# Optimization experiments

Hardware: AMD Instinct MI355X
Metric: run time of the kernel (lower is better)

The kernel has to match this reference:

```python
import jax, jax.numpy as jnp
import numpy as np

SHAPES = ((100, 100), (50, 50), (25, 25), (13, 13))
LENS = [h * w for h, w in SHAPES]
STARTS = [0]
for n in LENS[:-1]:
    STARTS.append(STARTS[-1] + n)
S_TOT = sum(LENS)  # 13294
B, C, HH, DH, L, P, NQ, NL, FF = 2, 256, 8, 32, 4, 4, 300, 6, 1024
WH = np.array([[w, h] for h, w in SHAPES], np.float32)  # [L,2] (W,H) offset normalizer


def ln(x, g, b):
    m = x.mean(-1, keepdims=True)
    v = ((x - m) ** 2).mean(-1, keepdims=True)
    return (x - m) * jax.lax.rsqrt(v + 1e-5) * g + b


def bilinear(v, grid):
    # v: [N,Hl,Wl,D]; grid: [N,Q,2] in [-1,1]; grid_sample bilinear, align_corners=False, zero padding
    N, Hl, Wl, Dd = v.shape
    x = (grid[..., 0] + 1.0) * 0.5 * Wl - 0.5
    y = (grid[..., 1] + 1.0) * 0.5 * Hl - 0.5
    x0f = jnp.floor(x); y0f = jnp.floor(y)
    wx = x - x0f; wy = y - y0f
    x0 = x0f.astype(jnp.int32); y0 = y0f.astype(jnp.int32)
    vf = v.reshape(N, Hl * Wl, Dd)
    def g(yi, xi):
        valid = (yi >= 0) & (yi < Hl) & (xi >= 0) & (xi < Wl)
        idx = jnp.clip(yi, 0, Hl - 1) * Wl + jnp.clip(xi, 0, Wl - 1)
        return jnp.take_along_axis(vf, idx[..., None], axis=1) * valid[..., None]
    return (((1 - wy) * (1 - wx))[..., None] * g(y0, x0)
            + ((1 - wy) * wx)[..., None] * g(y0, x0 + 1)
            + (wy * (1 - wx))[..., None] * g(y0 + 1, x0)
            + (wy * wx)[..., None] * g(y0 + 1, x0 + 1))


def msda(query, ref, src, so_w, so_b, aw_w, aw_b, vp_w, vp_b, op_w, op_b):
    # query:[B,Lq,C] ref:[B,Lq,L,2] src:[B,S,C]
    Bq, Lq, _ = query.shape
    value = (src @ vp_w.T + vp_b).reshape(Bq, S_TOT, HH, DH)
    offs = (query @ so_w.T + so_b).reshape(Bq, Lq, HH, L, P, 2)
    aw = jax.nn.softmax((query @ aw_w.T + aw_b).reshape(Bq, Lq, HH, L * P), -1)
    aw = aw.reshape(Bq, Lq, HH, L, P)
    loc = ref[:, :, None, :, None, :] + offs / jnp.asarray(WH)[None, None, None, :, None, :]
    grid = 2.0 * loc - 1.0  # [B,Lq,HH,L,P,2]
    out = jnp.zeros((Bq, HH, Lq, DH), query.dtype)
    for l, (Hl, Wl) in enumerate(SHAPES):
        st = STARTS[l]
        v_l = value[:, st:st + Hl * Wl].reshape(Bq, Hl, Wl, HH, DH).transpose(0, 3, 1, 2, 4).reshape(Bq * HH, Hl, Wl, DH)
        g_l = grid[:, :, :, l].transpose(0, 2, 1, 3, 4).reshape(Bq * HH, Lq * P, 2)
        s = bilinear(v_l, g_l).reshape(Bq, HH, Lq, P, DH)
        out = out + jnp.einsum('bqhp,bhqpd->bhqd', aw[:, :, :, l], s)
    out = out.transpose(0, 2, 1, 3).reshape(Bq, Lq, C)
    return out @ op_w.T + op_b


def enc_ref_points():
    refs = []
    for Hl, Wl in SHAPES:
        ry = (jnp.arange(Hl, dtype=jnp.float32) + 0.5) / Hl
        rx = (jnp.arange(Wl, dtype=jnp.float32) + 0.5) / Wl
        gy, gx = jnp.meshgrid(ry, rx, indexing='ij')
        refs.append(jnp.stack([gx.reshape(-1), gy.reshape(-1)], -1))
    r = jnp.concatenate(refs, 0)  # [S,2]; valid_ratios == 1 (no padding)
    return jnp.broadcast_to(r[None, :, None, :], (B, S_TOT, L, 2))


def _forward(src_flatten, pos_flatten, query_embed, level_embed, refp_w, refp_b,
             eso_w, eso_b, eaw_w, eaw_b, evp_w, evp_b, eop_w, eop_b,
             en1_g, en1_b, el1_w, el1_b, el2_w, el2_b, en2_g, en2_b,
             dso_w, dso_b, daw_w, daw_b, dvp_w, dvp_b, dop_w, dop_b,
             dsa_in_w, dsa_in_b, dsa_out_w, dsa_out_b,
             dn1_g, dn1_b, dn2_g, dn2_b, dn3_g, dn3_b,
             dl1_w, dl1_b, dl2_w, dl2_b):
    lev = jnp.concatenate([jnp.broadcast_to(level_embed[l], (LENS[l], C)) for l in range(L)], 0)
    pos = pos_flatten + lev[None]
    memory = src_flatten
    eref = enc_ref_points()
    for i in range(NL):  # encoder
        q = memory + pos
        m2 = msda(q, eref, memory, eso_w[i], eso_b[i], eaw_w[i], eaw_b[i], evp_w[i], evp_b[i], eop_w[i], eop_b[i])
        memory = ln(memory + m2, en1_g[i], en1_b[i])
        f = jax.nn.relu(memory @ el1_w[i].T + el1_b[i]) @ el2_w[i].T + el2_b[i]
        memory = ln(memory + f, en2_g[i], en2_b[i])
    qpos, tgt = jnp.split(query_embed, 2, axis=-1)
    qpos = jnp.broadcast_to(qpos[None], (B, NQ, C))
    tgt = jnp.broadcast_to(tgt[None], (B, NQ, C))
    ref = jax.nn.sigmoid(qpos @ refp_w.T + refp_b)  # [B,NQ,2]
    init_ref = ref
    ref_in = jnp.broadcast_to(ref[:, :, None, :], (B, NQ, L, 2))
    scale = 1.0 / np.sqrt(DH)
    for i in range(NL):  # decoder
        q = tgt + qpos
        wq, wk, wv = jnp.split(dsa_in_w[i], 3, 0)
        bq, bk, bv = jnp.split(dsa_in_b[i], 3, 0)
        qh = (q @ wq.T + bq).reshape(B, NQ, HH, DH).transpose(0, 2, 1, 3)
        kh = (q @ wk.T + bk).reshape(B, NQ, HH, DH).transpose(0, 2, 1, 3)
        vh = (tgt @ wv.T + bv).reshape(B, NQ, HH, DH).transpose(0, 2, 1, 3)
        att = jax.nn.softmax(jnp.einsum('bhqd,bhkd->bhqk', qh, kh) * scale, -1)
        sa = jnp.einsum('bhqk,bhkd->bhqd', att, vh).transpose(0, 2, 1, 3).reshape(B, NQ, C)
        sa = sa @ dsa_out_w[i].T + dsa_out_b[i]
        tgt = ln(tgt + sa, dn2_g[i], dn2_b[i])
        ca = msda(tgt + qpos, ref_in, memory, dso_w[i], dso_b[i], daw_w[i], daw_b[i], dvp_w[i], dvp_b[i], dop_w[i], dop_b[i])
        tgt = ln(tgt + ca, dn1_g[i], dn1_b[i])
        f = jax.nn.relu(tgt @ dl1_w[i].T + dl1_b[i]) @ dl2_w[i].T + dl2_b[i]
        tgt = ln(tgt + f, dn3_g[i], dn3_b[i])
    return tgt, init_ref, ref


def setup_inputs() -> dict:
    ks = iter(jax.random.split(jax.random.key(0), 80))
    def rn(shape, s=0.02):
        return jax.random.normal(next(ks), shape, jnp.float32) * s
    z = lambda shape: jnp.zeros(shape, jnp.float32)
    o = lambda shape: jnp.ones(shape, jnp.float32)
    HLP2, HLP = HH * L * P * 2, HH * L * P
    return {
        'src_flatten': rn((B, S_TOT, C), 1.0),
        'pos_flatten': rn((B, S_TOT, C), 1.0),
        'query_embed': rn((NQ, 2 * C), 1.0),
        'level_embed': rn((L, C), 1.0),
        'refp_w': rn((2, C)), 'refp_b': z((2,)),
        'eso_w': rn((NL, HLP2, C)), 'eso_b': z((NL, HLP2)),
        'eaw_w': rn((NL, HLP, C)), 'eaw_b': z((NL, HLP)),
        'evp_w': rn((NL, C, C)), 'evp_b': z((NL, C)),
        'eop_w': rn((NL, C, C)), 'eop_b': z((NL, C)),
        'en1_g': o((NL, C)), 'en1_b': z((NL, C)),
        'el1_w': rn((NL, FF, C)), 'el1_b': z((NL, FF)),
        'el2_w': rn((NL, C, FF)), 'el2_b': z((NL, C)),
        'en2_g': o((NL, C)), 'en2_b': z((NL, C)),
        'dso_w': rn((NL, HLP2, C)), 'dso_b': z((NL, HLP2)),
        'daw_w': rn((NL, HLP, C)), 'daw_b': z((NL, HLP)),
        'dvp_w': rn((NL, C, C)), 'dvp_b': z((NL, C)),
        'dop_w': rn((NL, C, C)), 'dop_b': z((NL, C)),
        'dsa_in_w': rn((NL, 3 * C, C)), 'dsa_in_b': z((NL, 3 * C)),
        'dsa_out_w': rn((NL, C, C)), 'dsa_out_b': z((NL, C)),
        'dn1_g': o((NL, C)), 'dn1_b': z((NL, C)),
        'dn2_g': o((NL, C)), 'dn2_b': z((NL, C)),
        'dn3_g': o((NL, C)), 'dn3_b': z((NL, C)),
        'dl1_w': rn((NL, FF, C)), 'dl1_b': z((NL, FF)),
        'dl2_w': rn((NL, C, FF)), 'dl2_b': z((NL, C)),
    }


def reference(src_flatten, pos_flatten, query_embed, level_embed, refp_w, refp_b,
              eso_w, eso_b, eaw_w, eaw_b, evp_w, evp_b, eop_w, eop_b,
              en1_g, en1_b, el1_w, el1_b, el2_w, el2_b, en2_g, en2_b,
              dso_w, dso_b, daw_w, daw_b, dvp_w, dvp_b, dop_w, dop_b,
              dsa_in_w, dsa_in_b, dsa_out_w, dsa_out_b,
              dn1_g, dn1_b, dn2_g, dn2_b, dn3_g, dn3_b,
              dl1_w, dl1_b, dl2_w, dl2_b):
    return _forward(src_flatten, pos_flatten, query_embed, level_embed, refp_w, refp_b,
                    eso_w, eso_b, eaw_w, eaw_b, evp_w, evp_b, eop_w, eop_b,
                    en1_g, en1_b, el1_w, el1_b, el2_w, el2_b, en2_g, en2_b,
                    dso_w, dso_b, daw_w, daw_b, dvp_w, dvp_b, dop_w, dop_b,
                    dsa_in_w, dsa_in_b, dsa_out_w, dsa_out_b,
                    dn1_g, dn1_b, dn2_g, dn2_b, dn3_g, dn3_b,
                    dl1_w, dl1_b, dl2_w, dl2_b)
```

## Files before the change

### kernel.cpp

```cpp
#include <hip/hip_runtime.h>

static constexpr int kS  = 13294;
static constexpr int kB  = 2;
static constexpr int kBS = kB * kS;
static constexpr int kC  = 256;
static constexpr int kH  = 8;
static constexpr int kNQ = 300;
static constexpr int kFF = 1024;
static constexpr int kNL = 6;

using short8 = __attribute__((ext_vector_type(8))) short;
using f32x4  = __attribute__((ext_vector_type(4))) float;

__device__ __forceinline__ unsigned short f2b(float f) {
  unsigned u = __builtin_bit_cast(unsigned, f);
  return (unsigned short)((u + 0x7FFF + ((u >> 16) & 1)) >> 16);
}
__device__ __forceinline__ float bf2f(unsigned short u) {
  return __builtin_bit_cast(float, ((unsigned)u) << 16);
}

#if defined(__has_builtin)
#if __has_builtin(__builtin_amdgcn_global_load_lds)
#define HAS_GLL 1
#endif
#endif
#ifndef HAS_GLL
#define HAS_GLL 0
#endif

#if HAS_GLL
typedef const __attribute__((address_space(1))) void* gas_t;
typedef __attribute__((address_space(3))) void* las_t;
#define GLOAD16(gp, lp) __builtin_amdgcn_global_load_lds((gas_t)(gp), (las_t)(lp), 16, 0, 0)
#endif

template<int ACT, int OBF>
__global__ __launch_bounds__(256) void gemm_mfma(
    const unsigned short* __restrict__ A,
    const unsigned short* __restrict__ Wt,
    const float* __restrict__ bias,
    void* __restrict__ outp,
    int M, int N, int K) {
  __shared__ __align__(16) unsigned short As[128 * 64];
  __shared__ __align__(16) unsigned short Bs[128 * 64];
  const int t = threadIdx.x;
  const int m0 = blockIdx.y * 128, n0 = blockIdx.x * 128;
  const int wid = t >> 6, lane = t & 63;
  const int wr = wid >> 1, wc = wid & 1;
  const int srow = t >> 3;
  const int scol = (t & 7) * 8;
  const int lr = lane & 15;
  const int lk = (lane >> 4) * 8;

  f32x4 acc[4][4];
#pragma unroll
  for (int i = 0; i < 4; ++i)
#pragma unroll
    for (int j = 0; j < 4; ++j) acc[i][j] = (f32x4){0.f, 0.f, 0.f, 0.f};

  for (int k0 = 0; k0 < K; k0 += 64) {
#if HAS_GLL
    __syncthreads();
#pragma unroll
    for (int c = 0; c < 4; ++c) {
      int ar = m0 + c * 32 + srow; if (ar >= M) ar = M - 1;
      GLOAD16(A + (size_t)ar * K + k0 + scol, (char*)As + c * 4096 + t * 16);
      int br = n0 + c * 32 + srow; if (br >= N) br = N - 1;
      GLOAD16(Wt + (size_t)br * K + k0 + scol, (char*)Bs + c * 4096 + t * 16);
    }
    __syncthreads();
#else
    short8 ta[4], tb[4];
#pragma unroll
    for (int c = 0; c < 4; ++c) {
      int ar = m0 + c * 32 + srow; if (ar >= M) ar = M - 1;
      ta[c] = *(const short8*)(A + (size_t)ar * K + k0 + scol);
      int br = n0 + c * 32 + srow; if (br >= N) br = N - 1;
      tb[c] = *(const short8*)(Wt + (size_t)br * K + k0 + scol);
    }
    __syncthreads();
#pragma unroll
    for (int c = 0; c < 4; ++c) {
      *(short8*)&As[c * 2048 + t * 8] = ta[c];
      *(short8*)&Bs[c * 2048 + t * 8] = tb[c];
    }
    __syncthreads();
#endif
#pragma unroll
    for (int kk = 0; kk < 2; ++kk) {
      short8 af[4], bf[4];
#pragma unroll
      for (int mi = 0; mi < 4; ++mi)
        af[mi] = *(const short8*)&As[(wr * 64 + mi * 16 + lr) * 64 + kk * 32 + lk];
#pragma unroll
      for (int ni = 0; ni < 4; ++ni)
        bf[ni] = *(const short8*)&Bs[(wc * 64 + ni * 16 + lr) * 64 + kk * 32 + lk];
#pragma unroll
      for (int mi = 0; mi < 4; ++mi)
#pragma unroll
        for (int ni = 0; ni < 4; ++ni)
          acc[mi][ni] = __builtin_amdgcn_mfma_f32_16x16x32_bf16(af[mi], bf[ni], acc[mi][ni], 0, 0, 0);
    }
  }
  const int orow0 = m0 + wr * 64;
  const int ocol = n0 + wc * 64 + (lane & 15);
  float bv[4];
#pragma unroll
  for (int ni = 0; ni < 4; ++ni) bv[ni] = bias[ocol + ni * 16];
#pragma unroll
  for (int mi = 0; mi < 4; ++mi) {
#pragma unroll
    for (int j = 0; j < 4; ++j) {
      const int r = orow0 + mi * 16 + (lane >> 4) * 4 + j;
      if (r < M) {
#pragma unroll
        for (int ni = 0; ni < 4; ++ni) {
          float v = acc[mi][ni][j] + bv[ni];
          if (ACT) v = fmaxf(v, 0.f);
          if (OBF) ((unsigned short*)outp)[(size_t)r * N + ocol + ni * 16] = f2b(v);
          else     ((float*)outp)[(size_t)r * N + ocol + ni * 16] = v;
        }
      }
    }
  }
}

template<int ACT, int OBF>
__global__ __launch_bounds__(256) void gemm_mfma_s(
    const unsigned short* __restrict__ A, const unsigned short* __restrict__ Wt,
    const float* __restrict__ bias, void* __restrict__ outp, int M, int N, int K) {
  __shared__ __align__(16) unsigned short As[64 * 64];
  __shared__ __align__(16) unsigned short Bs[64 * 64];
  const int t = threadIdx.x;
  const int m0 = blockIdx.y * 64, n0 = blockIdx.x * 64;
  const int wid = t >> 6, lane = t & 63;
  const int wr = wid >> 1, wc = wid & 1;
  const int srow = t >> 3;
  const int scol = (t & 7) * 8;
  const int lr = lane & 15;
  const int lk = (lane >> 4) * 8;

  f32x4 acc[2][2];
#pragma unroll
  for (int i = 0; i < 2; ++i)
#pragma unroll
    for (int j = 0; j < 2; ++j) acc[i][j] = (f32x4){0.f, 0.f, 0.f, 0.f};

  for (int k0 = 0; k0 < K; k0 += 64) {
#if HAS_GLL
    __syncthreads();
#pragma unroll
    for (int c = 0; c < 2; ++c) {
      int ar = m0 + c * 32 + srow; if (ar >= M) ar = M - 1;
      GLOAD16(A + (size_t)ar * K + k0 + scol, (char*)As + c * 4096 + t * 16);
      int br = n0 + c * 32 + srow; if (br >= N) br = N - 1;
      GLOAD16(Wt + (size_t)br * K + k0 + scol, (char*)Bs + c * 4096 + t * 16);
    }
    __syncthreads();
#else
    short8 ta[2], tb[2];
#pragma unroll
    for (int c = 0; c < 2; ++c) {
      int ar = m0 + c * 32 + srow; if (ar >= M) ar = M - 1;
      ta[c] = *(const short8*)(A + (size_t)ar * K + k0 + scol);
      int br = n0 + c * 32 + srow; if (br >= N) br = N - 1;
      tb[c] = *(const short8*)(Wt + (size_t)br * K + k0 + scol);
    }
    __syncthreads();
#pragma unroll
    for (int c = 0; c < 2; ++c) {
      *(short8*)&As[c * 2048 + t * 8] = ta[c];
      *(short8*)&Bs[c * 2048 + t * 8] = tb[c];
    }
    __syncthreads();
#endif
#pragma unroll
    for (int kk = 0; kk < 2; ++kk) {
      short8 af[2], bf[2];
#pragma unroll
      for (int mi = 0; mi < 2; ++mi)
        af[mi] = *(const short8*)&As[(wr * 32 + mi * 16 + lr) * 64 + kk * 32 + lk];
#pragma unroll
      for (int ni = 0; ni < 2; ++ni)
        bf[ni] = *(const short8*)&Bs[(wc * 32 + ni * 16 + lr) * 64 + kk * 32 + lk];
#pragma unroll
      for (int mi = 0; mi < 2; ++mi)
#pragma unroll
        for (int ni = 0; ni < 2; ++ni)
          acc[mi][ni] = __builtin_amdgcn_mfma_f32_16x16x32_bf16(af[mi], bf[ni], acc[mi][ni], 0, 0, 0);
    }
  }
  const int orow0 = m0 + wr * 32;
  const int ocol = n0 + wc * 32 + (lane & 15);
  float bv[2];
#pragma unroll
  for (int ni = 0; ni < 2; ++ni) bv[ni] = bias[ocol + ni * 16];
#pragma unroll
  for (int mi = 0; mi < 2; ++mi) {
#pragma unroll
    for (int j = 0; j < 4; ++j) {
      const int r = orow0 + mi * 16 + (lane >> 4) * 4 + j;
      if (r < M) {
#pragma unroll
        for (int ni = 0; ni < 2; ++ni) {
          float v = acc[mi][ni][j] + bv[ni];
          if (ACT) v = fmaxf(v, 0.f);
          if (OBF) ((unsigned short*)outp)[(size_t)r * N + ocol + ni * 16] = f2b(v);
          else     ((float*)outp)[(size_t)r * N + ocol + ni * 16] = v;
        }
      }
    }
  }
}

__global__ void cast_bf_k(const float* __restrict__ in, unsigned short* __restrict__ out, int n4) {
  int i = blockIdx.x * 256 + threadIdx.x;
  if (i >= n4) return;
  float4 v = ((const float4*)in)[i];
  ushort4 o; o.x = f2b(v.x); o.y = f2b(v.y); o.z = f2b(v.z); o.w = f2b(v.w);
  ((ushort4*)out)[i] = o;
}

__global__ void copy_cast_k(const float* __restrict__ in, float* __restrict__ outf,
                            unsigned short* __restrict__ outb, int n4) {
  int i = blockIdx.x * 256 + threadIdx.x;
  if (i >= n4) return;
  float4 v = ((const float4*)in)[i];
  ((float4*)outf)[i] = v;
  ushort4 o; o.x = f2b(v.x); o.y = f2b(v.y); o.z = f2b(v.z); o.w = f2b(v.w);
  ((ushort4*)outb)[i] = o;
}

__global__ void pack_bias_k(const float* __restrict__ so_b, const float* __restrict__ aw_b,
                            float* __restrict__ fb) {
  int i = blockIdx.x * 256 + threadIdx.x;
  if (i >= kNL * 384) return;
  int l = i / 384, j = i - l * 384;
  fb[i] = (j < 256) ? so_b[l * 256 + j] : aw_b[l * 128 + j - 256];
}

__global__ void enc_q_k(const float* __restrict__ mem, const float* __restrict__ pos,
                        const float* __restrict__ lev, unsigned short* __restrict__ q, int n4) {
  int i = blockIdx.x * 256 + threadIdx.x;
  if (i >= n4) return;
  int c4 = i & 63;
  int row = i >> 6;
  int s = row % kS;
  int l = (s < 10000) ? 0 : (s < 12500) ? 1 : (s < 13125) ? 2 : 3;
  float4 m = ((const float4*)mem)[i];
  float4 p = ((const float4*)pos)[i];
  float4 lv = ((const float4*)(lev + l * kC))[c4];
  ushort4 o;
  o.x = f2b(m.x + p.x + lv.x); o.y = f2b(m.y + p.y + lv.y);
  o.z = f2b(m.z + p.z + lv.z); o.w = f2b(m.w + p.w + lv.w);
  ((ushort4*)q)[i] = o;
}

__global__ void refs_k(float* __restrict__ refS) {
  int s = blockIdx.x * 256 + threadIdx.x;
  if (s >= kS) return;
  int st, W;
  if (s < 10000)      { st = 0;     W = 100; }
  else if (s < 12500) { st = 10000; W = 50; }
  else if (s < 13125) { st = 12500; W = 25; }
  else                { st = 13125; W = 13; }
  int idx = s - st;
  int y = idx / W;
  int x = idx - y * W;
  refS[s * 2 + 0] = (x + 0.5f) / (float)W;
  refS[s * 2 + 1] = (y + 0.5f) / (float)W;
}

__global__ __launch_bounds__(256) void msda_fused_k(
    const unsigned short* __restrict__ value, const float* __restrict__ foab,
    const float* __restrict__ refs, unsigned short* __restrict__ out, int Mq) {
  __shared__ int   sidx[2][kH][16][4];
  __shared__ float sw[2][kH][16][4];
  const int t = threadIdx.x;
  const int bq0 = blockIdx.x * 2;
  {
    const int qq = t >> 7;
    const int bq = bq0 + qq;
    const int b = (bq >= Mq) ? 1 : 0;
    const int qi = bq - b * Mq;
    const int h = (t >> 4) & 7, lp = t & 15, l = lp >> 2;
    const float* row = foab + (size_t)bq * 384;
    float logit = row[256 + h * 16 + lp];
    float mx = logit;
#pragma unroll
    for (int o = 1; o < 16; o <<= 1) mx = fmaxf(mx, __shfl_xor(mx, o));
    float e = __expf(logit - mx), ssum = e;
#pragma unroll
    for (int o = 1; o < 16; o <<= 1) ssum += __shfl_xor(ssum, o);
    const float a = e / ssum;
    const float offx = row[h * 32 + lp * 2];
    const float offy = row[h * 32 + lp * 2 + 1];
    const float rx = refs[qi * 2 + 0];
    const float ry = refs[qi * 2 + 1];
    const int wtab[4] = {100, 50, 25, 13};
    const int stab[4] = {0, 10000, 12500, 13125};
    const int W = wtab[l];
    const int start = stab[l];
    const float px = fmaf(rx, (float)W, offx) - 0.5f;
    const float py = fmaf(ry, (float)W, offy) - 0.5f;
    const float fx = floorf(px), fy = floorf(py);
    const float wx = px - fx, wy = py - fy;
    const int x0 = (int)fx, y0 = (int)fy;
    const int x0c = min(max(x0, 0), W - 1);
    const int x1c = min(max(x0 + 1, 0), W - 1);
    const int y0c = min(max(y0, 0), W - 1);
    const int y1c = min(max(y0 + 1, 0), W - 1);
    const float vx0 = (x0 >= 0 && x0 < W) ? 1.f : 0.f;
    const float vx1 = (x0 + 1 >= 0 && x0 + 1 < W) ? 1.f : 0.f;
    const float vy0 = (y0 >= 0 && y0 < W) ? 1.f : 0.f;
    const float vy1 = (y0 + 1 >= 0 && y0 + 1 < W) ? 1.f : 0.f;
    sidx[qq][h][lp][0] = (start + y0c * W + x0c) * 512;
    sidx[qq][h][lp][1] = (start + y0c * W + x1c) * 512;
    sidx[qq][h][lp][2] = (start + y1c * W + x0c) * 512;
    sidx[qq][h][lp][3] = (start + y1c * W + x1c) * 512;
    const float omwx = 1.f - wx, omwy = 1.f - wy;
    sw[qq][h][lp][0] = a * omwy * omwx * vy0 * vx0;
    sw[qq][h][lp][1] = a * omwy * wx * vy0 * vx1;
    sw[qq][h][lp][2] = a * wy * omwx * vy1 * vx0;
    sw[qq][h][lp][3] = a * wy * wx * vy1 * vx1;
  }
  __syncthreads();
  const int h = t >> 5, d = t & 31;
  const int chan = (h * 32 + d) * 2;
#pragma unroll
  for (int qq = 0; qq < 2; ++qq) {
    const int bq = bq0 + qq;
    const int b = (bq >= Mq) ? 1 : 0;
    const char* base = (const char*)value + (size_t)b * kS * 512;
    float acc0 = 0.f, acc1 = 0.f, acc2 = 0.f, acc3 = 0.f;
#pragma unroll
    for (int p0 = 0; p0 < 16; p0 += 8) {
      float vv[32], ww[32];
#pragma unroll
      for (int pp = 0; pp < 8; ++pp) {
        const int4 I = *(const int4*)&sidx[qq][h][p0 + pp][0];
        const float4 Wv = *(const float4*)&sw[qq][h][p0 + pp][0];
        vv[pp * 4 + 0] = bf2f(*(const unsigned short*)(base + I.x + chan));
        vv[pp * 4 + 1] = bf2f(*(const unsigned short*)(base + I.y + chan));
        vv[pp * 4 + 2] = bf2f(*(const unsigned short*)(base + I.z + chan));
        vv[pp * 4 + 3] = bf2f(*(const unsigned short*)(base + I.w + chan));
        ww[pp * 4 + 0] = Wv.x; ww[pp * 4 + 1] = Wv.y;
        ww[pp * 4 + 2] = Wv.z; ww[pp * 4 + 3] = Wv.w;
      }
#pragma unroll
      for (int j = 0; j < 32; j += 4) {
        acc0 = fmaf(ww[j + 0], vv[j + 0], acc0);
        acc1 = fmaf(ww[j + 1], vv[j + 1], acc1);
        acc2 = fmaf(ww[j + 2], vv[j + 2], acc2);
        acc3 = fmaf(ww[j + 3], vv[j + 3], acc3);
      }
    }
    out[((size_t)bq * 8 + h) * 32 + d] = f2b((acc0 + acc1) + (acc2 + acc3));
  }
}

__global__ __launch_bounds__(256) void ln_res_k(
    const float* __restrict__ x, const float* __restrict__ y,
    const float* __restrict__ g, const float* __restrict__ be,
    float* __restrict__ out, unsigned short* __restrict__ out_bf, int rows) {
  const int wid = threadIdx.x >> 6;
  const int lane = threadIdx.x & 63;
  const int row = blockIdx.x * 4 + wid;
  if (row >= rows) return;
  const float4 a = ((const float4*)(x + (size_t)row * 256))[lane];
  const float4 b = ((const float4*)(y + (size_t)row * 256))[lane];
  const float v0 = a.x + b.x, v1 = a.y + b.y, v2 = a.z + b.z, v3 = a.w + b.w;
  float s = v0 + v1 + v2 + v3;
  float s2 = v0 * v0 + v1 * v1 + v2 * v2 + v3 * v3;
#pragma unroll
  for (int off = 32; off; off >>= 1) {
    s += __shfl_xor(s, off);
    s2 += __shfl_xor(s2, off);
  }
  const float mean = s * (1.f / 256.f);
  const float var = s2 * (1.f / 256.f) - mean * mean;
  const float r = rsqrtf(var + 1e-5f);
  const float4 gg = ((const float4*)g)[lane];
  const float4 bb = ((const float4*)be)[lane];
  float4 o;
  o.x = (v0 - mean) * r * gg.x + bb.x;
  o.y = (v1 - mean) * r * gg.y + bb.y;
  o.z = (v2 - mean) * r * gg.z + bb.z;
  o.w = (v3 - mean) * r * gg.w + bb.w;
  ((float4*)(out + (size_t)row * 256))[lane] = o;
  ushort4 ob; ob.x = f2b(o.x); ob.y = f2b(o.y); ob.z = f2b(o.z); ob.w = f2b(o.w);
  ((ushort4*)(out_bf + (size_t)row * 256))[lane] = ob;
}

__global__ void add_bcast_bf_k(const float* __restrict__ a, const float* __restrict__ b,
                               unsigned short* __restrict__ out, int n4, int nb4) {
  int i = blockIdx.x * 256 + threadIdx.x;
  if (i >= n4) return;
  const float4 av = ((const float4*)a)[i];
  const float4 bv = ((const float4*)b)[i % nb4];
  ushort4 o;
  o.x = f2b(av.x + bv.x); o.y = f2b(av.y + bv.y);
  o.z = f2b(av.z + bv.z); o.w = f2b(av.w + bv.w);
  ((ushort4*)out)[i] = o;
}

__global__ void dec_init_k(const float* __restrict__ qe, float* __restrict__ tgt,
                           unsigned short* __restrict__ tgt_bf, float* __restrict__ qposb) {
  int i = blockIdx.x * 256 + threadIdx.x;
  if (i >= kNQ * kC) return;
  int q = i >> 8, c = i & 255;
  qposb[i] = qe[q * 512 + c];
  float tg = qe[q * 512 + 256 + c];
  tgt[i] = tg;
  tgt[kNQ * kC + i] = tg;
  unsigned short tb = f2b(tg);
  tgt_bf[i] = tb;
  tgt_bf[kNQ * kC + i] = tb;
}

__global__ __launch_bounds__(64) void ref_k(const float* __restrict__ qposb,
                                            const float* __restrict__ rw,
                                            const float* __restrict__ rb,
                                            float* __restrict__ ref300) {
  const int q = blockIdx.x;
  const int lane = threadIdx.x;
  const float4 qv = ((const float4*)(qposb + q * 256))[lane];
  const float4 w0 = ((const float4*)rw)[lane];
  const float4 w1 = ((const float4*)(rw + 256))[lane];
  float a0 = qv.x * w0.x + qv.y * w0.y + qv.z * w0.z + qv.w * w0.w;
  float a1 = qv.x * w1.x + qv.y * w1.y + qv.z * w1.z + qv.w * w1.w;
#pragma unroll
  for (int off = 32; off; off >>= 1) {
    a0 += __shfl_xor(a0, off);
    a1 += __shfl_xor(a1, off);
  }
  if (lane == 0) {
    ref300[q * 2 + 0] = 1.f / (1.f + __expf(-(a0 + rb[0])));
    ref300[q * 2 + 1] = 1.f / (1.f + __expf(-(a1 + rb[1])));
  }
}

__global__ __launch_bounds__(64) void dec_attn_k(const float* __restrict__ qk,
                                                 const float* __restrict__ v,
                                                 unsigned short* __restrict__ outp) {
  const int bid = blockIdx.x;
  const int q = bid % kNQ;
  const int bh = bid / kNQ;
  const int h = bh & 7;
  const int b = bh >> 3;
  const int lane = threadIdx.x;
  __shared__ float p[304];
  const float* qv = qk + ((size_t)(b * kNQ + q)) * 512 + h * 32;
  float qreg[32];
#pragma unroll
  for (int m = 0; m < 32; ++m) qreg[m] = qv[m];
  float scores[5];
  float mx = -1e30f;
#pragma unroll
  for (int j = 0; j < 5; ++j) {
    const int k = lane + j * 64;
    float sc = -1e30f;
    if (k < kNQ) {
      const float* kv = qk + ((size_t)(b * kNQ + k)) * 512 + 256 + h * 32;
      float acc = 0.f;
#pragma unroll
      for (int m = 0; m < 32; ++m) acc = fmaf(qreg[m], kv[m], acc);
      sc = acc * 0.17677669529663687f;
    }
    scores[j] = sc;
    mx = fmaxf(mx, sc);
  }
#pragma unroll
  for (int off = 32; off; off >>= 1) mx = fmaxf(mx, __shfl_xor(mx, off));
  float sum = 0.f;
// ... 10 lines not shown
  const float inv = 1.f / sum;
#pragma unroll
  for (int j = 0; j < 5; ++j) {
    const int k = lane + j * 64;
    if (k < kNQ) p[k] = scores[j] * inv;
  }
  __syncthreads();
  const int d = lane & 31, half = lane >> 5;
  float acc = 0.f;
  for (int k = half * 150; k < half * 150 + 150; ++k)
    acc = fmaf(p[k], v[((size_t)(b * kNQ + k)) * 256 + h * 32 + d], acc);
  acc += __shfl_down(acc, 32);
  if (lane < 32) outp[((size_t)(b * kNQ + q)) * 256 + h * 32 + d] = f2b(acc);
}

__global__ void write_refs_k(const float* __restrict__ ref300, float* __restrict__ outp) {
  int i = blockIdx.x * 256 + threadIdx.x;
  if (i >= 1200) return;
  float v = ref300[i % 600];
  outp[153600 + i] = v;
  outp[154800 + i] = v;
}

__global__ void sentinel_k(float* __restrict__ outp) {
  if (threadIdx.x < 64) outp[threadIdx.x] = 12345.0f;
}

extern "C" void kernel_launch(void* const* d_in, const int* in_sizes, int n_in,
                              void* d_out, int out_size, void* d_ws, size_t ws_size,
                              hipStream_t stream) {
  const float* src      = (const float*)d_in[0];
  const float* pos      = (const float*)d_in[1];
  const float* qe       = (const float*)d_in[2];
  const float* lev      = (const float*)d_in[3];
  const float* refp_w   = (const float*)d_in[4];
  const float* refp_b   = (const float*)d_in[5];
  const float* eso_w    = (const float*)d_in[6];
  const float* eso_b    = (const float*)d_in[7];
  const float* eaw_w    = (const float*)d_in[8];
  const float* eaw_b    = (const float*)d_in[9];
  const float* evp_w    = (const float*)d_in[10];
  const float* evp_b    = (const float*)d_in[11];
  const float* eop_w    = (const float*)d_in[12];
  const float* eop_b    = (const float*)d_in[13];
  const float* en1_g    = (const float*)d_in[14];
  const float* en1_b    = (const float*)d_in[15];
  const float* el1_w    = (const float*)d_in[16];
  const float* el1_b    = (const float*)d_in[17];
  const float* el2_w    = (const float*)d_in[18];
  const float* el2_b    = (const float*)d_in[19];
  const float* en2_g    = (const float*)d_in[20];
  const float* en2_b    = (const float*)d_in[21];
  const float* dso_w    = (const float*)d_in[22];
  const float* dso_b    = (const float*)d_in[23];
  const float* daw_w    = (const float*)d_in[24];
  const float* daw_b    = (const float*)d_in[25];
  const float* dvp_w    = (const float*)d_in[26];
  const float* dvp_b    = (const float*)d_in[27];
  const float* dop_w    = (const float*)d_in[28];
  const float* dop_b    = (const float*)d_in[29];
  const float* dsa_in_w = (const float*)d_in[30];
  const float* dsa_in_b = (const float*)d_in[31];
  const float* dsa_out_w= (const float*)d_in[32];
  const float* dsa_out_b= (const float*)d_in[33];
  const float* dn1_g    = (const float*)d_in[34];
  const float* dn1_b    = (const float*)d_in[35];
  const float* dn2_g    = (const float*)d_in[36];
  const float* dn2_b    = (const float*)d_in[37];
  const float* dn3_g    = (const float*)d_in[38];
  const float* dn3_b    = (const float*)d_in[39];
  const float* dl1_w    = (const float*)d_in[40];
  const float* dl1_b    = (const float*)d_in[41];
  const float* dl2_w    = (const float*)d_in[42];
  const float* dl2_b    = (const float*)d_in[43];

  float* Wsp = (float*)d_ws;
  size_t off = 0;
  auto alloc = [&](size_t n) { float* p = Wsp + off; off += n; return p; };
  const size_t NBC = (size_t)kBS * kC;
  float* memory   = alloc(NBC);
  unsigned short* memory_bf = (unsigned short*)alloc(NBC / 2);
  float* r2       = alloc(NBC);
  unsigned short* val_bf = (unsigned short*)r2;
  float* ffn2out  = r2;
  float* r3       = alloc(NBC / 2);
  unsigned short* qbuf_bf = (unsigned short*)r3;
  unsigned short* sampbuf_bf = (unsigned short*)r3;
  float* r4       = alloc(NBC * 2);
  float* foab     = r4;
  float* msdabuf  = r4;
  unsigned short* hid_bf = (unsigned short*)r4;
  float* refS     = alloc((size_t)kS * 2 + 2);
  auto allocb = [&](size_t elems) { return (unsigned short*)alloc(elems / 2); };
  unsigned short* fesoawW = allocb((size_t)kNL * 384 * 256);
  unsigned short* evpW  = allocb((size_t)kNL * 65536);
  unsigned short* eopW  = allocb((size_t)kNL * 65536);
  unsigned short* el1W  = allocb((size_t)kNL * 262144);
  unsigned short* el2W  = allocb((size_t)kNL * 262144);
  unsigned short* fdsoawW = allocb((size_t)kNL * 384 * 256);
  unsigned short* dvpW  = allocb((size_t)kNL * 65536);
  unsigned short* dopW  = allocb((size_t)kNL * 65536);
  unsigned short* dsaiW = allocb((size_t)kNL * 196608);
  unsigned short* dsaoW = allocb((size_t)kNL * 65536);
  unsigned short* dl1W  = allocb((size_t)kNL * 262144);
  unsigned short* dl2W  = allocb((size_t)kNL * 262144);
  float* fbias_e  = alloc((size_t)kNL * 384);
  float* fbias_d  = alloc((size_t)kNL * 384);
  const size_t NQC = (size_t)kB * kNQ * kC;
  float* tgt      = alloc(NQC);
  unsigned short* tgt_bf = (unsigned short*)alloc(NQC / 2);
  float* qposb    = alloc((size_t)kNQ * kC);
  unsigned short* dq_bf = (unsigned short*)alloc(NQC / 2);
  float* qkbuf    = alloc(NQC * 2);
  float* vbuf     = alloc(NQC);
  unsigned short* sabuf_bf = (unsigned short*)alloc(NQC / 2);
  float* sa2buf   = alloc(NQC);
  float* dfoab    = alloc((size_t)kB * kNQ * 384);
  unsigned short* dsamp_bf = (unsigned short*)alloc(NQC / 2);
  float* dmsda    = alloc(NQC);
  unsigned short* dffnh_bf = (unsigned short*)alloc((size_t)kB * kNQ * kFF / 2);
  float* dffn     = alloc(NQC);
  float* ref300   = alloc(600);

  if (ws_size < off * sizeof(float)) {
    hipLaunchKernelGGL(sentinel_k, dim3(1), dim3(64), 0, stream, (float*)d_out);
    return;
  }

  auto GEMM = [&](const unsigned short* A, const unsigned short* Wt, const float* bias,
                  void* out, int M, int N, int K, int variant) {
    dim3 g(N / 128, (M + 127) / 128);
    if (variant == 1)
      hipLaunchKernelGGL((gemm_mfma<1, 1>), g, dim3(256), 0, stream, A, Wt, bias, out, M, N, K);
    else if (variant == 2)
      hipLaunchKernelGGL((gemm_mfma<0, 1>), g, dim3(256), 0, stream, A, Wt, bias, out, M, N, K);
    else
      hipLaunchKernelGGL((gemm_mfma<0, 0>), g, dim3(256), 0, stream, A, Wt, bias, out, M, N, K);
  };
  auto GEMMS = [&](const unsigned short* A, const unsigned short* Wt, const float* bias,
                   void* out, int M, int N, int K, int variant) {
    dim3 g(N / 64, (M + 63) / 64);
    if (variant == 1)
      hipLaunchKernelGGL((gemm_mfma_s<1, 1>), g, dim3(256), 0, stream, A, Wt, bias, out, M, N, K);
    else if (variant == 2)
      hipLaunchKernelGGL((gemm_mfma_s<0, 1>), g, dim3(256), 0, stream, A, Wt, bias, out, M, N, K);
    else
      hipLaunchKernelGGL((gemm_mfma_s<0, 0>), g, dim3(256), 0, stream, A, Wt, bias, out, M, N, K);
  };
  auto CASTW = [&](const float* srcw, unsigned short* dstw, size_t elems) {
    int n4 = (int)(elems / 4);
    hipLaunchKernelGGL(cast_bf_k, dim3((n4 + 255) / 256), dim3(256), 0, stream, srcw, dstw, n4);
  };

  for (int i = 0; i < kNL; ++i) {
    CASTW(eso_w + (size_t)i * 65536, fesoawW + (size_t)i * 98304, 65536);
    CASTW(eaw_w + (size_t)i * 32768, fesoawW + (size_t)i * 98304 + 65536, 32768);
    CASTW(dso_w + (size_t)i * 65536, fdsoawW + (size_t)i * 98304, 65536);
    CASTW(daw_w + (size_t)i * 32768, fdsoawW + (size_t)i * 98304 + 65536, 32768);
  }
  CASTW(evp_w, evpW, (size_t)kNL * 65536);
  CASTW(eop_w, eopW, (size_t)kNL * 65536);
  CASTW(el1_w, el1W, (size_t)kNL * 262144);
  CASTW(el2_w, el2W, (size_t)kNL * 262144);
  CASTW(dvp_w, dvpW, (size_t)kNL * 65536);
  CASTW(dop_w, dopW, (size_t)kNL * 65536);
  CASTW(dsa_in_w, dsaiW, (size_t)kNL * 196608);
  CASTW(dsa_out_w, dsaoW, (size_t)kNL * 65536);
  CASTW(dl1_w, dl1W, (size_t)kNL * 262144);
  CASTW(dl2_w, dl2W, (size_t)kNL * 262144);
  hipLaunchKernelGGL(pack_bias_k, dim3((kNL * 384 + 255) / 256), dim3(256), 0, stream,
                     eso_b, eaw_b, fbias_e);
  hipLaunchKernelGGL(pack_bias_k, dim3((kNL * 384 + 255) / 256), dim3(256), 0, stream,
                     dso_b, daw_b, fbias_d);
  const int n4full = kBS * 64;
  hipLaunchKernelGGL(copy_cast_k, dim3((n4full + 255) / 256), dim3(256), 0, stream,
                     src, memory, memory_bf, n4full);
  hipLaunchKernelGGL(refs_k, dim3((kS + 255) / 256), dim3(256), 0, stream, refS);

  for (int i = 0; i < kNL; ++i) {
    hipLaunchKernelGGL(enc_q_k, dim3((n4full + 255) / 256), dim3(256), 0, stream,
                       memory, pos, lev, qbuf_bf, n4full);
    GEMM(memory_bf, evpW + (size_t)i * 65536, evp_b + i * kC, val_bf, kBS, 256, 256, 2);
    GEMM(qbuf_bf, fesoawW + (size_t)i * 98304, fbias_e + i * 384, foab, kBS, 384, 256, 0);
    hipLaunchKernelGGL(msda_fused_k, dim3(kBS / 2), dim3(256), 0, stream,
                       val_bf, foab, refS, sampbuf_bf, kS);
    GEMM(sampbuf_bf, eopW + (size_t)i * 65536, eop_b + i * kC, msdabuf, kBS, 256, 256, 0);
    hipLaunchKernelGGL(ln_res_k, dim3(kBS / 4), dim3(256), 0, stream,
                       memory, msdabuf, en1_g + i * kC, en1_b + i * kC, memory, memory_bf, kBS);
    GEMM(memory_bf, el1W + (size_t)i * 262144, el1_b + i * kFF, hid_bf, kBS, 1024, 256, 1);
    GEMM(hid_bf, el2W + (size_t)i * 262144, el2_b + i * kC, ffn2out, kBS, 256, 1024, 0);
    hipLaunchKernelGGL(ln_res_k, dim3(kBS / 4), dim3(256), 0, stream,
                       memory, ffn2out, en2_g + i * kC, en2_b + i * kC, memory, memory_bf, kBS);
  }

  hipLaunchKernelGGL(dec_init_k, dim3(300), dim3(256), 0, stream, qe, tgt, tgt_bf, qposb);
  hipLaunchKernelGGL(ref_k, dim3(kNQ), dim3(64), 0, stream, qposb, refp_w, refp_b, ref300);

  const int dn4 = kB * kNQ * 64;
  const int qn4 = kNQ * 64;
  const int MD = kB * kNQ;
  for (int i = 0; i < kNL; ++i) {
    hipLaunchKernelGGL(add_bcast_bf_k, dim3((dn4 + 255) / 256), dim3(256), 0, stream,
                       tgt, qposb, dq_bf, dn4, qn4);
    GEMMS(dq_bf, dsaiW + (size_t)i * 196608, dsa_in_b + i * 768, qkbuf, MD, 512, 256, 0);
    GEMMS(tgt_bf, dsaiW + (size_t)i * 196608 + (size_t)512 * 256,
          dsa_in_b + i * 768 + 512, vbuf, MD, 256, 256, 0);
    hipLaunchKernelGGL(dec_attn_k, dim3(kB * kH * kNQ), dim3(64), 0, stream,
                       qkbuf, vbuf, sabuf_bf);
    GEMMS(sabuf_bf, dsaoW + (size_t)i * 65536, dsa_out_b + i * kC, sa2buf, MD, 256, 256, 0);
    hipLaunchKernelGGL(ln_res_k, dim3((MD + 3) / 4), dim3(256), 0, stream,
                       tgt, sa2buf, dn2_g + i * kC, dn2_b + i * kC, tgt, tgt_bf, MD);
    hipLaunchKernelGGL(add_bcast_bf_k, dim3((dn4 + 255) / 256), dim3(256), 0, stream,
                       tgt, qposb, dq_bf, dn4, qn4);
    GEMM(memory_bf, dvpW + (size_t)i * 65536, dvp_b + i * kC, val_bf, kBS, 256, 256, 2);
    GEMMS(dq_bf, fdsoawW + (size_t)i * 98304, fbias_d + i * 384, dfoab, MD, 384, 256, 0);
    hipLaunchKernelGGL(msda_fused_k, dim3(MD / 2), dim3(256), 0, stream,
                       val_bf, dfoab, ref300, dsamp_bf, kNQ);
    GEMMS(dsamp_bf, dopW + (size_t)i * 65536, dop_b + i * kC, dmsda, MD, 256, 256, 0);
    hipLaunchKernelGGL(ln_res_k, dim3((MD + 3) / 4), dim3(256), 0, stream,
                       tgt, dmsda, dn1_g + i * kC, dn1_b + i * kC, tgt, tgt_bf, MD);
    GEMMS(tgt_bf, dl1W + (size_t)i * 262144, dl1_b + i * kFF, dffnh_bf, MD, 1024, 256, 1);
    GEMMS(dffnh_bf, dl2W + (size_t)i * 262144, dl2_b + i * kC, dffn, MD, 256, 1024, 0);
    hipLaunchKernelGGL(ln_res_k, dim3((MD + 3) / 4), dim3(256), 0, stream,
                       tgt, dffn, dn3_g + i * kC, dn3_b + i * kC, tgt, tgt_bf, MD);
  }

  hipMemcpyAsync(d_out, tgt, NQC * sizeof(float), hipMemcpyDeviceToDevice, stream);
  hipLaunchKernelGGL(write_refs_k, dim3(5), dim3(256), 0, stream, ref300, (float*)d_out);
}
```

Before: 2.104 ms.

## Fuse GEMM with residual LayerNorm, batch decoder value projections, vectorize MSDA gathers

Adds a gemm_ln_k kernel that computes a full 256-wide output row block and applies bias, residual add and LayerNorm in its epilogue. The encoder variant also writes the next layer's query (memory + pos + level embed), which removes the separate ln_res and enc_q passes and their fp32 intermediate round-trips. The six decoder value projections are computed once as a single wide GEMM before the decoder loop, and MSDA reads them through a configurable stride and column offset. The MSDA gather now loads two bf16 channels per 32-bit access. The trade-off is lower parallelism, since there is one 64-row block per 256 columns, plus a larger value buffer and more strided gather traffic in the decoder.

```diff
diff --git a/kernel.cpp b/kernel.cpp
--- a/kernel.cpp
+++ b/kernel.cpp
@@ -16,8 +16,11 @@
   unsigned u = __builtin_bit_cast(unsigned, f);
   return (unsigned short)((u + 0x7FFF + ((u >> 16) & 1)) >> 16);
 }
-__device__ __forceinline__ float bf2f(unsigned short u) {
-  return __builtin_bit_cast(float, ((unsigned)u) << 16);
+__device__ __forceinline__ float bflo(unsigned u) {
+  return __builtin_bit_cast(float, u << 16);
+}
+__device__ __forceinline__ float bfhi(unsigned u) {
+  return __builtin_bit_cast(float, u & 0xFFFF0000u);
 }
 
 #if defined(__has_builtin)
@@ -37,11 +40,8 @@
 
 template<int ACT, int OBF>
 __global__ __launch_bounds__(256) void gemm_mfma(
-    const unsigned short* __restrict__ A,
-    const unsigned short* __restrict__ Wt,
-    const float* __restrict__ bias,
-    void* __restrict__ outp,
-    int M, int N, int K) {
+    const unsigned short* __restrict__ A, const unsigned short* __restrict__ Wt,
+    const float* __restrict__ bias, void* __restrict__ outp, int M, int N, int K) {
   __shared__ __align__(16) unsigned short As[128 * 64];
   __shared__ __align__(16) unsigned short Bs[128 * 64];
   const int t = threadIdx.x;
@@ -208,6 +208,148 @@
           if (ACT) v = fmaxf(v, 0.f);
           if (OBF) ((unsigned short*)outp)[(size_t)r * N + ocol + ni * 16] = f2b(v);
           else     ((float*)outp)[(size_t)r * N + ocol + ni * 16] = v;
+        }
+      }
+    }
+  }
+}
+
+template<int WRITEQ>
+__global__ __launch_bounds__(256) void gemm_ln_k(
+    const unsigned short* __restrict__ A, const unsigned short* __restrict__ Wt,
+    const float* __restrict__ bias, const float* __restrict__ x,
+    const float* __restrict__ g, const float* __restrict__ be,
+    float* __restrict__ outf, unsigned short* __restrict__ outb,
+    unsigned short* __restrict__ qout, const float* __restrict__ pos,
+    const float* __restrict__ lev, int M, int K) {
+  __shared__ __align__(16) unsigned short As[64 * 64];
+  __shared__ __align__(16) unsigned short Bs[256 * 64];
+  __shared__ float rsum[64][4], rsq[64][4], rmv[64][2];
+  const int t = threadIdx.x;
+  const int m0 = blockIdx.x * 64;
+  const int wid = t >> 6, lane = t & 63;
+  const int srow = t >> 3;
+  const int scol = (t & 7) * 8;
+  const int lr = lane & 15;
+  const int q4 = lane >> 4;
+  const int lk = q4 * 8;
+
+  f32x4 acc[4][4];
+#pragma unroll
+  for (int i = 0; i < 4; ++i)
+#pragma unroll
+    for (int j = 0; j < 4; ++j) acc[i][j] = (f32x4){0.f, 0.f, 0.f, 0.f};
+
+  for (int k0 = 0; k0 < K; k0 += 64) {
+#if HAS_GLL
+    __syncthreads();
+#pragma unroll
+    for (int c = 0; c < 2; ++c) {
+      int ar = m0 + c * 32 + srow; if (ar >= M) ar = M - 1;
+      GLOAD16(A + (size_t)ar * K + k0 + scol, (char*)As + c * 4096 + t * 16);
+    }
+#pragma unroll
+    for (int c = 0; c < 8; ++c) {
+      GLOAD16(Wt + (size_t)(c * 32 + srow) * K + k0 + scol, (char*)Bs + c * 4096 + t * 16);
+    }
+    __syncthreads();
+#else
+    short8 ta[2], tb[8];
+#pragma unroll
+    for (int c = 0; c < 2; ++c) {
+      int ar = m0 + c * 32 + srow; if (ar >= M) ar = M - 1;
+      ta[c] = *(const short8*)(A + (size_t)ar * K + k0 + scol);
+    }
+#pragma unroll
+    for (int c = 0; c < 8; ++c)
+      tb[c] = *(const short8*)(Wt + (size_t)(c * 32 + srow) * K + k0 + scol);
+    __syncthreads();
+#pragma unroll
+    for (int c = 0; c < 2; ++c) *(short8*)&As[c * 2048 + t * 8] = ta[c];
+#pragma unroll
+    for (int c = 0; c < 8; ++c) *(short8*)&Bs[c * 2048 + t * 8] = tb[c];
+    __syncthreads();
+#endif
+#pragma unroll
+    for (int kk = 0; kk < 2; ++kk) {
+      short8 af[4], bf[4];
+#pragma unroll
+      for (int mi = 0; mi < 4; ++mi)
+        af[mi] = *(const short8*)&As[(mi * 16 + lr) * 64 + kk * 32 + lk];
+#pragma unroll
+      for (int ni = 0; ni < 4; ++ni)
+        bf[ni] = *(const short8*)&Bs[(wid * 64 + ni * 16 + lr) * 64 + kk * 32 + lk];
+#pragma unroll
+      for (int mi = 0; mi < 4; ++mi)
+#pragma unroll
+        for (int ni = 0; ni < 4; ++ni)
+          acc[mi][ni] = __builtin_amdgcn_mfma_f32_16x16x32_bf16(af[mi], bf[ni], acc[mi][ni], 0, 0, 0);
+    }
+  }
+  float bv[4], gv[4], bev[4];
+  int cols[4];
+#pragma unroll
+  for (int ni = 0; ni < 4; ++ni) {
+    cols[ni] = wid * 64 + ni * 16 + lr;
+    bv[ni] = bias[cols[ni]];
+    gv[ni] = g[cols[ni]];
+    bev[ni] = be[cols[ni]];
+  }
+#pragma unroll
+  for (int mi = 0; mi < 4; ++mi) {
+#pragma unroll
+    for (int j = 0; j < 4; ++j) {
+      const int brow = mi * 16 + q4 * 4 + j;
+      int grow = m0 + brow; if (grow >= M) grow = M - 1;
+      const float* xr = x + (size_t)grow * 256;
+      float s = 0.f, s2 = 0.f;
+#pragma unroll
+      for (int ni = 0; ni < 4; ++ni) {
+        float v = acc[mi][ni][j] + bv[ni] + xr[cols[ni]];
+        acc[mi][ni][j] = v;
+        s += v; s2 += v * v;
+      }
+#pragma unroll
+      for (int o = 1; o < 16; o <<= 1) {
+        s += __shfl_xor(s, o);
+        s2 += __shfl_xor(s2, o);
+      }
+      if (lr == 0) { rsum[brow][wid] = s; rsq[brow][wid] = s2; }
+    }
+  }
+  __syncthreads();
+  if (t < 64) {
+    float s = rsum[t][0] + rsum[t][1] + rsum[t][2] + rsum[t][3];
+    float s2 = rsq[t][0] + rsq[t][1] + rsq[t][2] + rsq[t][3];
+    float mean = s * (1.f / 256.f);
+    float var = s2 * (1.f / 256.f) - mean * mean;
+    rmv[t][0] = mean;
+    rmv[t][1] = rsqrtf(var + 1e-5f);
+  }
+  __syncthreads();
+#pragma unroll
+  for (int mi = 0; mi < 4; ++mi) {
+#pragma unroll
+    for (int j = 0; j < 4; ++j) {
+      const int brow = mi * 16 + q4 * 4 + j;
+      const int grow = m0 + brow;
+      if (grow >= M) continue;
+      const float mean = rmv[brow][0], rs = rmv[brow][1];
+      int levl = 0;
+      int srow_g = grow;
+      if (WRITEQ) {
+        srow_g = (grow >= kS) ? grow - kS : grow;
+        levl = (srow_g < 10000) ? 0 : (srow_g < 12500) ? 1 : (srow_g < 13125) ? 2 : 3;
+      }
+#pragma unroll
+      for (int ni = 0; ni < 4; ++ni) {
+        const float v = (acc[mi][ni][j] - mean) * rs * gv[ni] + bev[ni];
+        const size_t oi = (size_t)grow * 256 + cols[ni];
+        outf[oi] = v;
+        outb[oi] = f2b(v);
+        if (WRITEQ) {
+          const float qv = v + pos[oi] + lev[levl * 256 + cols[ni]];
+          qout[oi] = f2b(qv);
         }
       }
     }
@@ -273,14 +415,15 @@
 }
 
 __global__ __launch_bounds__(256) void msda_fused_k(
-    const unsigned short* __restrict__ value, const float* __restrict__ foab,
-    const float* __restrict__ refs, unsigned short* __restrict__ out, int Mq) {
+    const unsigned short* __restrict__ value, int vstride, int vcol,
+    const float* __restrict__ foab, const float* __restrict__ refs,
+    unsigned short* __restrict__ out, int Mq) {
   __shared__ int   sidx[2][kH][16][4];
   __shared__ float sw[2][kH][16][4];
   const int t = threadIdx.x;
   const int bq0 = blockIdx.x * 2;
+  const int qq = t >> 7;
   {
-    const int qq = t >> 7;
     const int bq = bq0 + qq;
     const int b = (bq >= Mq) ? 1 : 0;
     const int qi = bq - b * Mq;
@@ -315,10 +458,10 @@
     const float vx1 = (x0 + 1 >= 0 && x0 + 1 < W) ? 1.f : 0.f;
     const float vy0 = (y0 >= 0 && y0 < W) ? 1.f : 0.f;
     const float vy1 = (y0 + 1 >= 0 && y0 + 1 < W) ? 1.f : 0.f;
-    sidx[qq][h][lp][0] = (start + y0c * W + x0c) * 512;
-    sidx[qq][h][lp][1] = (start + y0c * W + x1c) * 512;
-    sidx[qq][h][lp][2] = (start + y1c * W + x0c) * 512;
-    sidx[qq][h][lp][3] = (start + y1c * W + x1c) * 512;
+    sidx[qq][h][lp][0] = (start + y0c * W + x0c) * vstride + vcol;
+    sidx[qq][h][lp][1] = (start + y0c * W + x1c) * vstride + vcol;
+    sidx[qq][h][lp][2] = (start + y1c * W + x0c) * vstride + vcol;
+    sidx[qq][h][lp][3] = (start + y1c * W + x1c) * vstride + vcol;
     const float omwx = 1.f - wx, omwy = 1.f - wy;
     sw[qq][h][lp][0] = a * omwy * omwx * vy0 * vx0;
     sw[qq][h][lp][1] = a * omwy * wx * vy0 * vx1;
@@ -326,71 +469,38 @@
     sw[qq][h][lp][3] = a * wy * wx * vy1 * vx1;
   }
   __syncthreads();
-  const int h = t >> 5, d = t & 31;
-  const int chan = (h * 32 + d) * 2;
-#pragma unroll
-  for (int qq = 0; qq < 2; ++qq) {
-    const int bq = bq0 + qq;
-    const int b = (bq >= Mq) ? 1 : 0;
-    const char* base = (const char*)value + (size_t)b * kS * 512;
-    float acc0 = 0.f, acc1 = 0.f, acc2 = 0.f, acc3 = 0.f;
-#pragma unroll
-    for (int p0 = 0; p0 < 16; p0 += 8) {
-      float vv[32], ww[32];
-#pragma unroll
-      for (int pp = 0; pp < 8; ++pp) {
-        const int4 I = *(const int4*)&sidx[qq][h][p0 + pp][0];
-        const float4 Wv = *(const float4*)&sw[qq][h][p0 + pp][0];
-        vv[pp * 4 + 0] = bf2f(*(const unsigned short*)(base + I.x + chan));
-        vv[pp * 4 + 1] = bf2f(*(const unsigned short*)(base + I.y + chan));
-        vv[pp * 4 + 2] = bf2f(*(const unsigned short*)(base + I.z + chan));
-        vv[pp * 4 + 3] = bf2f(*(const unsigned short*)(base + I.w + chan));
-        ww[pp * 4 + 0] = Wv.x; ww[pp * 4 + 1] = Wv.y;
-        ww[pp * 4 + 2] = Wv.z; ww[pp * 4 + 3] = Wv.w;
-      }
-#pragma unroll
-      for (int j = 0; j < 32; j += 4) {
-        acc0 = fmaf(ww[j + 0], vv[j + 0], acc0);
-        acc1 = fmaf(ww[j + 1], vv[j + 1], acc1);
-        acc2 = fmaf(ww[j + 2], vv[j + 2], acc2);
-        acc3 = fmaf(ww[j + 3], vv[j + 3], acc3);
-      }
-    }
-    out[((size_t)bq * 8 + h) * 32 + d] = f2b((acc0 + acc1) + (acc2 + acc3));
-  }
-}
-
-__global__ __launch_bounds__(256) void ln_res_k(
-    const float* __restrict__ x, const float* __restrict__ y,
-    const float* __restrict__ g, const float* __restrict__ be,
-    float* __restrict__ out, unsigned short* __restrict__ out_bf, int rows) {
-  const int wid = threadIdx.x >> 6;
-  const int lane = threadIdx.x & 63;
-  const int row = blockIdx.x * 4 + wid;
-  if (row >= rows) return;
-  const float4 a = ((const float4*)(x + (size_t)row * 256))[lane];
-  const float4 b = ((const float4*)(y + (size_t)row * 256))[lane];
-  const float v0 = a.x + b.x, v1 = a.y + b.y, v2 = a.z + b.z, v3 = a.w + b.w;
-  float s = v0 + v1 + v2 + v3;
-  float s2 = v0 * v0 + v1 * v1 + v2 * v2 + v3 * v3;
-#pragma unroll
-  for (int off = 32; off; off >>= 1) {
-    s += __shfl_xor(s, off);
-    s2 += __shfl_xor(s2, off);
-  }
-  const float mean = s * (1.f / 256.f);
-  const float var = s2 * (1.f / 256.f) - mean * mean;
-  const float r = rsqrtf(var + 1e-5f);
-  const float4 gg = ((const float4*)g)[lane];
-  const float4 bb = ((const float4*)be)[lane];
-  float4 o;
-  o.x = (v0 - mean) * r * gg.x + bb.x;
-  o.y = (v1 - mean) * r * gg.y + bb.y;
-  o.z = (v2 - mean) * r * gg.z + bb.z;
-  o.w = (v3 - mean) * r * gg.w + bb.w;
-  ((float4*)(out + (size_t)row * 256))[lane] = o;
-  ushort4 ob; ob.x = f2b(o.x); ob.y = f2b(o.y); ob.z = f2b(o.z); ob.w = f2b(o.w);
-  ((ushort4*)(out_bf + (size_t)row * 256))[lane] = ob;
+  const int h = (t >> 4) & 7, dp = t & 15;
+  const int bq = bq0 + qq;
+  const int b = (bq >= Mq) ? 1 : 0;
+  const char* base = (const char*)value + (size_t)b * kS * vstride + (h * 64 + dp * 4);
+  float aLo0 = 0.f, aLo1 = 0.f, aHi0 = 0.f, aHi1 = 0.f;
+#pragma unroll
+  for (int p0 = 0; p0 < 16; p0 += 8) {
+    unsigned u[32];
+    float w[32];
+#pragma unroll
+    for (int pp = 0; pp < 8; ++pp) {
+      const int4 I = *(const int4*)&sidx[qq][h][p0 + pp][0];
+      const float4 Wv = *(const float4*)&sw[qq][h][p0 + pp][0];
+      u[pp * 4 + 0] = *(const unsigned*)(base + I.x);
+      u[pp * 4 + 1] = *(const unsigned*)(base + I.y);
+      u[pp * 4 + 2] = *(const unsigned*)(base + I.z);
+      u[pp * 4 + 3] = *(const unsigned*)(base + I.w);
+      w[pp * 4 + 0] = Wv.x; w[pp * 4 + 1] = Wv.y;
+      w[pp * 4 + 2] = Wv.z; w[pp * 4 + 3] = Wv.w;
+    }
+#pragma unroll
+    for (int j = 0; j < 32; j += 2) {
+      aLo0 = fmaf(w[j], bflo(u[j]), aLo0);
+      aHi0 = fmaf(w[j], bfhi(u[j]), aHi0);
+      aLo1 = fmaf(w[j + 1], bflo(u[j + 1]), aLo1);
+      aHi1 = fmaf(w[j + 1], bfhi(u[j + 1]), aHi1);
+    }
+  }
+  const float accLo = aLo0 + aLo1;
+  const float accHi = aHi0 + aHi1;
+  const unsigned packed = (unsigned)f2b(accLo) | ((unsigned)f2b(accHi) << 16);
+  ((unsigned*)out)[(size_t)bq * 128 + h * 16 + dp] = packed;
 }
 
 __global__ void add_bcast_bf_k(const float* __restrict__ a, const float* __restrict__ b,
@@ -567,14 +677,13 @@
   unsigned short* memory_bf = (unsigned short*)alloc(NBC / 2);
   float* r2       = alloc(NBC);
   unsigned short* val_bf = (unsigned short*)r2;
-  float* ffn2out  = r2;
   float* r3       = alloc(NBC / 2);
   unsigned short* qbuf_bf = (unsigned short*)r3;
   unsigned short* sampbuf_bf = (unsigned short*)r3;
   float* r4       = alloc(NBC * 2);
   float* foab     = r4;
-  float* msdabuf  = r4;
   unsigned short* hid_bf = (unsigned short*)r4;
+  unsigned short* val_all = (unsigned short*)r2;
   float* refS     = alloc((size_t)kS * 2 + 2);
   auto allocb = [&](size_t elems) { return (unsigned short*)alloc(elems / 2); };
   unsigned short* fesoawW = allocb((size_t)kNL * 384 * 256);
@@ -599,12 +708,9 @@
   float* qkbuf    = alloc(NQC * 2);
   float* vbuf     = alloc(NQC);
   unsigned short* sabuf_bf = (unsigned short*)alloc(NQC / 2);
-  float* sa2buf   = alloc(NQC);
   float* dfoab    = alloc((size_t)kB * kNQ * 384);
   unsigned short* dsamp_bf = (unsigned short*)alloc(NQC / 2);
-  float* dmsda    = alloc(NQC);
   unsigned short* dffnh_bf = (unsigned short*)alloc((size_t)kB * kNQ * kFF / 2);
-  float* dffn     = alloc(NQC);
   float* ref300   = alloc(600);
 
   if (ws_size < off * sizeof(float)) {
@@ -627,8 +733,6 @@
     dim3 g(N / 64, (M + 63) / 64);
     if (variant == 1)
       hipLaunchKernelGGL((gemm_mfma_s<1, 1>), g, dim3(256), 0, stream, A, Wt, bias, out, M, N, K);
-    else if (variant == 2)
-      hipLaunchKernelGGL((gemm_mfma_s<0, 1>), g, dim3(256), 0, stream, A, Wt, bias, out, M, N, K);
     else
       hipLaunchKernelGGL((gemm_mfma_s<0, 0>), g, dim3(256), 0, stream, A, Wt, bias, out, M, N, K);
   };
@@ -661,29 +765,35 @@
   hipLaunchKernelGGL(copy_cast_k, dim3((n4full + 255) / 256), dim3(256), 0, stream,
                      src, memory, memory_bf, n4full);
   hipLaunchKernelGGL(refs_k, dim3((kS + 255) / 256), dim3(256), 0, stream, refS);
-
+  hipLaunchKernelGGL(enc_q_k, dim3((n4full + 255) / 256), dim3(256), 0, stream,
+                     memory, pos, lev, qbuf_bf, n4full);
+
+  const int grid_ln = (kBS + 63) / 64;
   for (int i = 0; i < kNL; ++i) {
-    hipLaunchKernelGGL(enc_q_k, dim3((n4full + 255) / 256), dim3(256), 0, stream,
-                       memory, pos, lev, qbuf_bf, n4full);
     GEMM(memory_bf, evpW + (size_t)i * 65536, evp_b + i * kC, val_bf, kBS, 256, 256, 2);
     GEMM(qbuf_bf, fesoawW + (size_t)i * 98304, fbias_e + i * 384, foab, kBS, 384, 256, 0);
     hipLaunchKernelGGL(msda_fused_k, dim3(kBS / 2), dim3(256), 0, stream,
-                       val_bf, foab, refS, sampbuf_bf, kS);
-    GEMM(sampbuf_bf, eopW + (size_t)i * 65536, eop_b + i * kC, msdabuf, kBS, 256, 256, 0);
-    hipLaunchKernelGGL(ln_res_k, dim3(kBS / 4), dim3(256), 0, stream,
-                       memory, msdabuf, en1_g + i * kC, en1_b + i * kC, memory, memory_bf, kBS);
+                       val_bf, 512, 0, foab, refS, sampbuf_bf, kS);
+    hipLaunchKernelGGL((gemm_ln_k<0>), dim3(grid_ln), dim3(256), 0, stream,
+                       sampbuf_bf, eopW + (size_t)i * 65536, eop_b + i * kC,
+                       memory, en1_g + i * kC, en1_b + i * kC,
+                       memory, memory_bf, (unsigned short*)nullptr,
+                       (const float*)nullptr, (const float*)nullptr, kBS, 256);
     GEMM(memory_bf, el1W + (size_t)i * 262144, el1_b + i * kFF, hid_bf, kBS, 1024, 256, 1);
-    GEMM(hid_bf, el2W + (size_t)i * 262144, el2_b + i * kC, ffn2out, kBS, 256, 1024, 0);
-    hipLaunchKernelGGL(ln_res_k, dim3(kBS / 4), dim3(256), 0, stream,
-                       memory, ffn2out, en2_g + i * kC, en2_b + i * kC, memory, memory_bf, kBS);
+    hipLaunchKernelGGL((gemm_ln_k<1>), dim3(grid_ln), dim3(256), 0, stream,
+                       hid_bf, el2W + (size_t)i * 262144, el2_b + i * kC,
+                       memory, en2_g + i * kC, en2_b + i * kC,
+                       memory, memory_bf, qbuf_bf, pos, lev, kBS, 1024);
   }
 
   hipLaunchKernelGGL(dec_init_k, dim3(300), dim3(256), 0, stream, qe, tgt, tgt_bf, qposb);
   hipLaunchKernelGGL(ref_k, dim3(kNQ), dim3(64), 0, stream, qposb, refp_w, refp_b, ref300);
+  GEMM(memory_bf, dvpW, dvp_b, val_all, kBS, kNL * 256, 256, 2);
 
   const int dn4 = kB * kNQ * 64;
   const int qn4 = kNQ * 64;
   const int MD = kB * kNQ;
+  const int grid_lnd = (MD + 63) / 64;
   for (int i = 0; i < kNL; ++i) {
     hipLaunchKernelGGL(add_bcast_bf_k, dim3((dn4 + 255) / 256), dim3(256), 0, stream,
                        tgt, qposb, dq_bf, dn4, qn4);
@@ -692,22 +802,27 @@
           dsa_in_b + i * 768 + 512, vbuf, MD, 256, 256, 0);
     hipLaunchKernelGGL(dec_attn_k, dim3(kB * kH * kNQ), dim3(64), 0, stream,
                        qkbuf, vbuf, sabuf_bf);
-    GEMMS(sabuf_bf, dsaoW + (size_t)i * 65536, dsa_out_b + i * kC, sa2buf, MD, 256, 256, 0);
-    hipLaunchKernelGGL(ln_res_k, dim3((MD + 3) / 4), dim3(256), 0, stream,
-                       tgt, sa2buf, dn2_g + i * kC, dn2_b + i * kC, tgt, tgt_bf, MD);
+    hipLaunchKernelGGL((gemm_ln_k<0>), dim3(grid_lnd), dim3(256), 0, stream,
+                       sabuf_bf, dsaoW + (size_t)i * 65536, dsa_out_b + i * kC,
+                       tgt, dn2_g + i * kC, dn2_b + i * kC,
+                       tgt, tgt_bf, (unsigned short*)nullptr,
+                       (const float*)nullptr, (const float*)nullptr, MD, 256);
     hipLaunchKernelGGL(add_bcast_bf_k, dim3((dn4 + 255) / 256), dim3(256), 0, stream,
                        tgt, qposb, dq_bf, dn4, qn4);
-    GEMM(memory_bf, dvpW + (size_t)i * 65536, dvp_b + i * kC, val_bf, kBS, 256, 256, 2);
     GEMMS(dq_bf, fdsoawW + (size_t)i * 98304, fbias_d + i * 384, dfoab, MD, 384, 256, 0);
     hipLaunchKernelGGL(msda_fused_k, dim3(MD / 2), dim3(256), 0, stream,
-                       val_bf, dfoab, ref300, dsamp_bf, kNQ);
-    GEMMS(dsamp_bf, dopW + (size_t)i * 65536, dop_b + i * kC, dmsda, MD, 256, 256, 0);
-    hipLaunchKernelGGL(ln_res_k, dim3((MD + 3) / 4), dim3(256), 0, stream,
-                       tgt, dmsda, dn1_g + i * kC, dn1_b + i * kC, tgt, tgt_bf, MD);
+                       val_all, kNL * 512, i * 512, dfoab, ref300, dsamp_bf, kNQ);
+    hipLaunchKernelGGL((gemm_ln_k<0>), dim3(grid_lnd), dim3(256), 0, stream,
+                       dsamp_bf, dopW + (size_t)i * 65536, dop_b + i * kC,
+                       tgt, dn1_g + i * kC, dn1_b + i * kC,
+                       tgt, tgt_bf, (unsigned short*)nullptr,
+                       (const float*)nullptr, (const float*)nullptr, MD, 256);
     GEMMS(tgt_bf, dl1W + (size_t)i * 262144, dl1_b + i * kFF, dffnh_bf, MD, 1024, 256, 1);
-    GEMMS(dffnh_bf, dl2W + (size_t)i * 262144, dl2_b + i * kC, dffn, MD, 256, 1024, 0);
-    hipLaunchKernelGGL(ln_res_k, dim3((MD + 3) / 4), dim3(256), 0, stream,
-                       tgt, dffn, dn3_g + i * kC, dn3_b + i * kC, tgt, tgt_bf, MD);
+    hipLaunchKernelGGL((gemm_ln_k<0>), dim3(grid_lnd), dim3(256), 0, stream,
+                       dffnh_bf, dl2W + (size_t)i * 262144, dl2_b + i * kC,
+                       tgt, dn3_g + i * kC, dn3_b + i * kC,
+                       tgt, tgt_bf, (unsigned short*)nullptr,
+                       (const float*)nullptr, (const float*)nullptr, MD, 1024);
   }
 
   hipMemcpyAsync(d_out, tgt, NQC * sizeof(float), hipMemcpyDeviceToDevice, stream);
```

Result: no change. 2.132 ms (+1.4%).
